# Kernel optimization log

Measured on AMD Instinct MI355X. Metric: run time of the kernel, lower is better.

The kernel has to match this reference:

```python
import jax, jax.numpy as jnp
import numpy as np

B, I, D = 4096, 64, 128  # batch, input_size (groups), n_dim


def setup_inputs() -> dict:
    key = jax.random.key(0)
    ks = jax.random.split(key, 9)
    return {
        "X": jax.random.normal(ks[0], (B, I, 2), dtype=jnp.float32),
        "M": jax.random.uniform(ks[1], (B, I), dtype=jnp.float32),
        "h": jax.random.normal(ks[2], (B, I * D), dtype=jnp.float32),
        "W_r_d": jax.random.normal(ks[3], (I, 2, D), dtype=jnp.float32) * 0.1,
        "W_z_d": jax.random.normal(ks[4], (I, 2, D), dtype=jnp.float32) * 0.1,
        "W_h_d": jax.random.normal(ks[5], (I, 2, D), dtype=jnp.float32) * 0.1,
        "U_r_d": jax.random.normal(ks[6], (I, D, D), dtype=jnp.float32) * 0.05,
        "U_z_d": jax.random.normal(ks[7], (I, D, D), dtype=jnp.float32) * 0.05,
        "U_h_d": jax.random.normal(ks[8], (I, D, D), dtype=jnp.float32) * 0.05,
        "b_r_d": jnp.zeros((I, D), dtype=jnp.float32),
        "b_z_d": jnp.zeros((I, D), dtype=jnp.float32),
        "b_h_d": jnp.zeros((I, D), dtype=jnp.float32),
    }


def reference(X, M, h, W_r_d, W_z_d, W_h_d, U_r_d, U_z_d, U_h_d, b_r_d, b_z_d, b_h_d):
    Bn = X.shape[0]
    hr = h.reshape(Bn, I, D)                     # [B, I, D]
    Mm = M[:, :, None]                           # [B, I, 1]
    r = jax.nn.sigmoid(jnp.einsum('bij,ijk->bik', X, W_r_d)
                       + jnp.einsum('bij,ijk->bik', hr, U_r_d) + b_r_d)
    z = jax.nn.sigmoid(jnp.einsum('bij,ijk->bik', X, W_z_d)
                       + jnp.einsum('bij,ijk->bik', hr, U_z_d) + b_z_d)
    h_tilde = jnp.tanh(jnp.einsum('bij,ijk->bik', X, W_h_d)
                       + jnp.einsum('bij,ijk->bik', r * hr, U_h_d) + b_h_d)
    h_new = z * hr + (1.0 - z) * h_tilde
    h_out = hr * (1.0 - Mm) + h_new * Mm         # masked blend
    return h_out.reshape(Bn, I * D)
```

## Files before the change

kernel.cpp:

```cpp
#include <hip/hip_runtime.h>
#include <hip/hip_bf16.h>

#define II 64
#define DD 128
#define ID (II*DD)
#define NIT 16
#define RPT 16

typedef __attribute__((ext_vector_type(8))) short short8;
typedef __attribute__((ext_vector_type(4))) float f32x4;

__device__ __forceinline__ short f2bf(float x) {
    __hip_bfloat16 b = __float2bfloat16(x);
    return __builtin_bit_cast(short, b);
}
__device__ __forceinline__ float sigf(float x) {
    return __fdividef(1.0f, 1.0f + __expf(-x));
}
__device__ __forceinline__ float tanhfast(float x) {
    return __fdividef(2.0f, 1.0f + __expf(-2.0f * x)) - 1.0f;
}

__global__ void prep_U(const float* __restrict__ Ur, const float* __restrict__ Uz,
                       const float* __restrict__ Uh, short* __restrict__ out) {
    int bx = blockIdx.x;
    int nf = bx & 7;
    int kk = (bx >> 3) & 3;
    int i  = (bx >> 5) & 63;
    int g  = bx >> 11;
    int lane = threadIdx.x;
    int lr = lane & 15, lg = lane >> 4;
    const float* U = (g == 0) ? Ur : (g == 1) ? Uz : Uh;
    const float* src = U + (size_t)i * DD * DD + (size_t)(kk * 32 + lg * 8) * DD + nf * 16 + lr;
    short8 v;
#pragma unroll
    for (int e = 0; e < 8; ++e) v[e] = f2bf(src[(size_t)e * DD]);
    short8* dst = (short8*)out;
    dst[(size_t)bx * 64 + lane] = v;
}

__global__ __launch_bounds__(256, 2)
void gru_main(const float* __restrict__ X, const float* __restrict__ M,
              const float* __restrict__ h,
              const float* __restrict__ Wr, const float* __restrict__ Wz,
              const float* __restrict__ Wh,
              const float* __restrict__ br, const float* __restrict__ bz,
              const float* __restrict__ bh,
              const short* __restrict__ Ut, float* __restrict__ out) {
    const int b   = blockIdx.x;
    const int x   = b & 7;
    const int r   = b >> 3;
    const int i   = x * 8 + (r >> 4);
    const int tb  = r & 15;
    const int row0b = tb * (NIT * RPT);

    const int tid  = threadIdx.x;
    const int lane = tid & 63;
    const int wv   = tid >> 6;
    const int lr   = lane & 15;
    const int lg   = lane >> 4;
    const int colbase = wv * 32;

    __shared__ float hbuf[2][16 * 132];
    __shared__ short rhb[16 * 136];

    const short8* UtF = (const short8*)Ut;
    short8 Bf[3][4][2];
#pragma unroll
    for (int g = 0; g < 3; ++g)
#pragma unroll
        for (int kk = 0; kk < 4; ++kk)
#pragma unroll
            for (int nt = 0; nt < 2; ++nt)
                Bf[g][kk][nt] = UtF[(size_t)(g * 64 + i) * 2048 + kk * 512 + (2 * wv + nt) * 64 + lane];

    float wts[3][2][2], bias[3][2];
    {
        const float* Wg[3] = {Wr, Wz, Wh};
        const float* bg[3] = {br, bz, bh};
#pragma unroll
        for (int g = 0; g < 3; ++g)
#pragma unroll
            for (int nt = 0; nt < 2; ++nt) {
                int c = colbase + nt * 16 + lr;
                wts[g][nt][0] = Wg[g][(size_t)i * 256 + c];
                wts[g][nt][1] = Wg[g][(size_t)i * 256 + 128 + c];
                bias[g][nt]   = bg[g][(size_t)i * 128 + c];
            }
    }

    const float2* Xp = (const float2*)X;

    {
        const float* hb = h + (size_t)row0b * ID + (size_t)i * DD;
        f32x4 sA = *(const f32x4*)(hb + (size_t)(tid >> 5) * ID + (tid & 31) * 4);
        f32x4 sB = *(const f32x4*)(hb + (size_t)(8 + (tid >> 5)) * ID + (tid & 31) * 4);
        float* db = &hbuf[0][0];
        *(f32x4*)(db + (tid >> 5) * 132 + (tid & 31) * 4) = sA;
        *(f32x4*)(db + (8 + (tid >> 5)) * 132 + (tid & 31) * 4) = sB;
    }

    for (int t = 0; t < NIT; ++t) {
        const int r0 = row0b + t * RPT;
        const int nb = (t + 1) & 1;
        const bool more = (t + 1) < NIT;

        f32x4 sA, sB;
        if (more) {
            const float* hb = h + (size_t)(row0b + (t + 1) * RPT) * ID + (size_t)i * DD;
            sA = *(const f32x4*)(hb + (size_t)(tid >> 5) * ID + (tid & 31) * 4);
            sB = *(const f32x4*)(hb + (size_t)(8 + (tid >> 5)) * ID + (tid & 31) * 4);
        }

        __syncthreads();

        const float* cbuf = &hbuf[t & 1][0];

        f32x4 accr[2], accz[2], acch[2];
#pragma unroll
        for (int nt = 0; nt < 2; ++nt) {
            accr[nt] = (f32x4){0.f, 0.f, 0.f, 0.f};
            accz[nt] = (f32x4){0.f, 0.f, 0.f, 0.f};
            acch[nt] = (f32x4){0.f, 0.f, 0.f, 0.f};
        }
#pragma unroll
        for (int kk = 0; kk < 4; ++kk) {
            const float* ap = cbuf + lr * 132 + kk * 32 + lg * 8;
            f32x4 u0 = *(const f32x4*)ap;
            f32x4 u1 = *(const f32x4*)(ap + 4);
            short8 a;
#pragma unroll
            for (int e = 0; e < 4; ++e) { a[e] = f2bf(u0[e]); a[e + 4] = f2bf(u1[e]); }
#pragma unroll
            for (int nt = 0; nt < 2; ++nt) {
                accr[nt] = __builtin_amdgcn_mfma_f32_16x16x32_bf16(a, Bf[0][kk][nt], accr[nt], 0, 0, 0);
                accz[nt] = __builtin_amdgcn_mfma_f32_16x16x32_bf16(a, Bf[1][kk][nt], accz[nt], 0, 0, 0);
            }
        }

        float x0a[4], x1a[4], hva[2][4];
#pragma unroll
        for (int reg = 0; reg < 4; ++reg) {
            const int row  = lg * 4 + reg;
            const int grow = r0 + row;
            float2 xv = Xp[(size_t)grow * II + i];
            x0a[reg] = xv.x; x1a[reg] = xv.y;
#pragma unroll
            for (int nt = 0; nt < 2; ++nt) {
                const int c = colbase + nt * 16 + lr;
                float hv = cbuf[row * 132 + c];
                hva[nt][reg] = hv;
                float rv = sigf(accr[nt][reg] + x0a[reg] * wts[0][nt][0] + x1a[reg] * wts[0][nt][1] + bias[0][nt]);
                rhb[row * 136 + c] = f2bf(rv * hv);
                accz[nt][reg] = sigf(accz[nt][reg] + x0a[reg] * wts[1][nt][0] + x1a[reg] * wts[1][nt][1] + bias[1][nt]);
            }
        }

        __syncthreads();

        if (more) {
            float* db = &hbuf[nb][0];
            *(f32x4*)(db + (tid >> 5) * 132 + (tid & 31) * 4) = sA;
            *(f32x4*)(db + (8 + (tid >> 5)) * 132 + (tid & 31) * 4) = sB;
        }

#pragma unroll
        for (int kk = 0; kk < 4; ++kk) {
            short8 pa = *(const short8*)&rhb[lr * 136 + kk * 32 + lg * 8];
#pragma unroll
            for (int nt = 0; nt < 2; ++nt)
                acch[nt] = __builtin_amdgcn_mfma_f32_16x16x32_bf16(pa, Bf[2][kk][nt], acch[nt], 0, 0, 0);
        }

#pragma unroll
        for (int reg = 0; reg < 4; ++reg) {
            const int grow = r0 + lg * 4 + reg;
            const float mv = M[(size_t)grow * II + i];
#pragma unroll
            for (int nt = 0; nt < 2; ++nt) {
                const int c = colbase + nt * 16 + lr;
                float ht = tanhfast(acch[nt][reg] + x0a[reg] * wts[2][nt][0] + x1a[reg] * wts[2][nt][1] + bias[2][nt]);
                float zv = accz[nt][reg];
                float hv = hva[nt][reg];
                float hnew = zv * hv + (1.0f - zv) * ht;
                out[(size_t)grow * ID + (size_t)i * DD + c] = hv * (1.0f - mv) + hnew * mv;
            }
        }
    }
}

extern "C" void kernel_launch(void* const* d_in, const int* in_sizes, int n_in,
                              void* d_out, int out_size, void* d_ws, size_t ws_size,
                              hipStream_t stream) {
    const float* X  = (const float*)d_in[0];
    const float* M  = (const float*)d_in[1];
    const float* h  = (const float*)d_in[2];
    const float* Wr = (const float*)d_in[3];
    const float* Wz = (const float*)d_in[4];
    const float* Wh = (const float*)d_in[5];
    const float* Ur = (const float*)d_in[6];
    const float* Uz = (const float*)d_in[7];
    const float* Uh = (const float*)d_in[8];
    const float* br = (const float*)d_in[9];
    const float* bz = (const float*)d_in[10];
    const float* bh = (const float*)d_in[11];
    float* out = (float*)d_out;
    short* Ut  = (short*)d_ws;

    prep_U<<<3 * II * 4 * 8, 64, 0, stream>>>(Ur, Uz, Uh, Ut);
    gru_main<<<64 * 16, 256, 0, stream>>>(X, M, h, Wr, Wz, Wh, br, bz, bh, Ut, out);
}
```

Measured before the change: 315.8 us.

## Halve rows per block and prefetch X and M one iteration ahead

```diff
diff --git a/kernel.cpp b/kernel.cpp
--- a/kernel.cpp
+++ b/kernel.cpp
@@ -4,8 +4,9 @@
 #define II 64
 #define DD 128
 #define ID (II*DD)
-#define NIT 16
+#define NIT 8
 #define RPT 16
+#define BROWS (NIT*RPT)
 
 typedef __attribute__((ext_vector_type(8))) short short8;
 typedef __attribute__((ext_vector_type(4))) float f32x4;
@@ -50,9 +51,9 @@
     const int b   = blockIdx.x;
     const int x   = b & 7;
     const int r   = b >> 3;
-    const int i   = x * 8 + (r >> 4);
-    const int tb  = r & 15;
-    const int row0b = tb * (NIT * RPT);
+    const int i   = x * 8 + (r >> 5);
+    const int tb  = r & 31;
+    const int row0b = tb * BROWS;
 
     const int tid  = threadIdx.x;
     const int lane = tid & 63;
@@ -99,17 +100,32 @@
         *(f32x4*)(db + (tid >> 5) * 132 + (tid & 31) * 4) = sA;
         *(f32x4*)(db + (8 + (tid >> 5)) * 132 + (tid & 31) * 4) = sB;
     }
+    float px0[4], px1[4], pmv[4];
+#pragma unroll
+    for (int reg = 0; reg < 4; ++reg) {
+        const int grow = row0b + lg * 4 + reg;
+        float2 xv = Xp[(size_t)grow * II + i];
+        px0[reg] = xv.x; px1[reg] = xv.y;
+        pmv[reg] = M[(size_t)grow * II + i];
+    }
 
     for (int t = 0; t < NIT; ++t) {
-        const int r0 = row0b + t * RPT;
         const int nb = (t + 1) & 1;
         const bool more = (t + 1) < NIT;
 
         f32x4 sA, sB;
+        float nx0[4], nx1[4], nmv[4];
         if (more) {
             const float* hb = h + (size_t)(row0b + (t + 1) * RPT) * ID + (size_t)i * DD;
             sA = *(const f32x4*)(hb + (size_t)(tid >> 5) * ID + (tid & 31) * 4);
             sB = *(const f32x4*)(hb + (size_t)(8 + (tid >> 5)) * ID + (tid & 31) * 4);
+            const int rbase = row0b + (t + 1) * RPT + lg * 4;
+#pragma unroll
+            for (int reg = 0; reg < 4; ++reg) {
+                float2 xv = Xp[(size_t)(rbase + reg) * II + i];
+                nx0[reg] = xv.x; nx1[reg] = xv.y;
+                nmv[reg] = M[(size_t)(rbase + reg) * II + i];
+            }
         }
 
         __syncthreads();
@@ -138,21 +154,18 @@
             }
         }
 
-        float x0a[4], x1a[4], hva[2][4];
+        float hva[2][4];
 #pragma unroll
         for (int reg = 0; reg < 4; ++reg) {
-            const int row  = lg * 4 + reg;
-            const int grow = r0 + row;
-            float2 xv = Xp[(size_t)grow * II + i];
-            x0a[reg] = xv.x; x1a[reg] = xv.y;
+            const int row = lg * 4 + reg;
 #pragma unroll
             for (int nt = 0; nt < 2; ++nt) {
                 const int c = colbase + nt * 16 + lr;
                 float hv = cbuf[row * 132 + c];
                 hva[nt][reg] = hv;
-                float rv = sigf(accr[nt][reg] + x0a[reg] * wts[0][nt][0] + x1a[reg] * wts[0][nt][1] + bias[0][nt]);
+                float rv = sigf(accr[nt][reg] + px0[reg] * wts[0][nt][0] + px1[reg] * wts[0][nt][1] + bias[0][nt]);
                 rhb[row * 136 + c] = f2bf(rv * hv);
-                accz[nt][reg] = sigf(accz[nt][reg] + x0a[reg] * wts[1][nt][0] + x1a[reg] * wts[1][nt][1] + bias[1][nt]);
+                accz[nt][reg] = sigf(accz[nt][reg] + px0[reg] * wts[1][nt][0] + px1[reg] * wts[1][nt][1] + bias[1][nt]);
             }
         }
 
@@ -174,16 +187,23 @@
 
 #pragma unroll
         for (int reg = 0; reg < 4; ++reg) {
-            const int grow = r0 + lg * 4 + reg;
-            const float mv = M[(size_t)grow * II + i];
+            const int grow = row0b + t * RPT + lg * 4 + reg;
+            const float mv = pmv[reg];
 #pragma unroll
             for (int nt = 0; nt < 2; ++nt) {
                 const int c = colbase + nt * 16 + lr;
-                float ht = tanhfast(acch[nt][reg] + x0a[reg] * wts[2][nt][0] + x1a[reg] * wts[2][nt][1] + bias[2][nt]);
+                float ht = tanhfast(acch[nt][reg] + px0[reg] * wts[2][nt][0] + px1[reg] * wts[2][nt][1] + bias[2][nt]);
                 float zv = accz[nt][reg];
                 float hv = hva[nt][reg];
                 float hnew = zv * hv + (1.0f - zv) * ht;
                 out[(size_t)grow * ID + (size_t)i * DD + c] = hv * (1.0f - mv) + hnew * mv;
+            }
+        }
+
+        if (more) {
+#pragma unroll
+            for (int reg = 0; reg < 4; ++reg) {
+                px0[reg] = nx0[reg]; px1[reg] = nx1[reg]; pmv[reg] = nmv[reg];
             }
         }
     }
@@ -208,5 +228,5 @@
     short* Ut  = (short*)d_ws;
 
     prep_U<<<3 * II * 4 * 8, 64, 0, stream>>>(Ur, Uz, Uh, Ut);
-    gru_main<<<64 * 16, 256, 0, stream>>>(X, M, h, Wr, Wz, Wh, br, bz, bh, Ut, out);
-}
+    gru_main<<<64 * 32, 256, 0, stream>>>(X, M, h, Wr, Wz, Wh, br, bz, bh, Ut, out);
+}
```

Result: no change. 315.0 us (-0.2%).
